# Performance work log

Hardware: AMD Instinct MI355X
Metric: run time of the kernel (lower is better)

## Reference

```python
import jax, jax.numpy as jnp
import numpy as np

NHEADS = 16

def setup_inputs() -> dict:
    key = jax.random.key(0)
    ks = jax.random.split(key, 5)
    C = 1024
    d = C // NHEADS
    x  = jax.random.normal(ks[0], (2, 2048, C), dtype=jnp.float32)
    sc = 1.0 / np.sqrt(C)
    wq = jax.random.normal(ks[1], (C, C), dtype=jnp.float32) * sc
    wk = jax.random.normal(ks[2], (C, C), dtype=jnp.float32) * sc
    wv = jax.random.normal(ks[3], (C, C), dtype=jnp.float32) * sc
    wo = jax.random.normal(ks[4], (d, C), dtype=jnp.float32) * (1.0 / np.sqrt(d))
    return {"x": x, "wq": wq, "wk": wk, "wv": wv, "wo": wo}

def reference(x, wq, wk, wv, wo):
    B, T, C = x.shape
    H = NHEADS
    d = C // H

    def split_heads(y):
        return y.reshape(B, T, H, d).transpose(0, 2, 1, 3)  # [B,H,T,d]

    Q = split_heads(x @ wq)
    K = split_heads(x @ wk)
    V = split_heads(x @ wv)

    # scores[b,h,q,k]
    prod = jnp.einsum('bhqd,bhkd->bhqk', Q, K) / np.sqrt(d)

    # ALiBi bias: offset[h, q, k] = (k - q) * 2**(-8*(h+1)/H)
    idx = jnp.arange(T)
    slopes = jnp.exp2(-8.0 * (jnp.arange(H, dtype=jnp.float32) + 1.0) / H)
    bias = (idx[None, :] - idx[:, None]).astype(x.dtype) * slopes[:, None, None]
    prod = prod + bias[None]

    # causal tril mask: keep k <= q
    keep = idx[None, :] <= idx[:, None]  # [T_q, T_k]
    prod = jnp.where(keep[None, None], prod, -jnp.inf)

    # NOTE: original uses F.softmax(prod, 2) -> softmax over the QUERY axis.
    attention_weights = jax.nn.softmax(prod, axis=2)
    attention_output = jnp.einsum('bhqk,bhkd->bhqd', attention_weights, V)

    # per-head wo projection then sum over heads == (sum over heads) @ wo (linear)
    outputs = attention_output.sum(axis=1) @ wo  # [B,T,C]
    return x + outputs
```

## Files before the change

### kernel.cpp

```cpp
#include <hip/hip_runtime.h>
#include <math.h>

#define NB 2
#define NH 16
#define NT 2048
#define ND 64
#define NC 1024
#define L2E 1.44269504f

typedef __attribute__((ext_vector_type(4))) float f32x4;
typedef __attribute__((ext_vector_type(8))) short short8;
typedef __attribute__((ext_vector_type(4))) short short4_t;
typedef __attribute__((ext_vector_type(8))) unsigned short ushort8;
typedef __attribute__((ext_vector_type(4))) unsigned short ushort4_t;

#define GLOAD_LDS(gp, lp)                                                \
    __builtin_amdgcn_global_load_lds(                                    \
        (const __attribute__((address_space(1))) void*)(gp),             \
        (__attribute__((address_space(3))) void*)(lp), 16, 0, 0)

__device__ __forceinline__ int sigma_p(int p) {
    return 4 * ((p >> 3) & 3) + (p & 3) + 16 * ((p >> 2) & 1) + 32 * (p >> 5);
}

__device__ __forceinline__ unsigned short f2bf(float f) {
    unsigned u = __builtin_bit_cast(unsigned, f);
    unsigned r = (u + 0x7FFFu + ((u >> 16) & 1u)) >> 16;
    return (unsigned short)r;
}

__device__ __forceinline__ unsigned cvtpk_bf16(float lo, float hi) {
    unsigned r;
    asm("v_cvt_pk_bf16_f32 %0, %1, %2" : "=v"(r) : "v"(lo), "v"(hi));
    return r;
}

__device__ __forceinline__ f32x4 mfma16(short8 a, short8 b, f32x4 c) {
    return __builtin_amdgcn_mfma_f32_16x16x32_bf16(a, b, c, 0, 0, 0);
}

__device__ __forceinline__ short8 frag_load(const unsigned short* rowp, int g, int half) {
    short8 v;
    short4_t lo = *(const short4_t*)(rowp + 4 * g + 32 * half);
    short4_t hi = *(const short4_t*)(rowp + 4 * g + 16 + 32 * half);
    #pragma unroll
    for (int j = 0; j < 4; ++j) { v[j] = lo[j]; v[4 + j] = hi[j]; }
    return v;
}

__device__ __forceinline__ short8 frag_g(const unsigned short* rowp, int g, int half) {
    return *(const short8*)(rowp + 8 * g + 32 * half);
}

__device__ __forceinline__ short8 frag_swz128(const unsigned short* tile, int row, int g, int half) {
    const char* p = (const char*)tile + row * 128 + (((g + 4 * half) ^ (row & 7)) << 4);
    return *(const short8*)p;
}

__global__ __launch_bounds__(256) void cvt_x(const float* __restrict__ src,
                                             unsigned short* __restrict__ dst, int n4) {
    int i = blockIdx.x * 256 + threadIdx.x;
    if (i >= n4) return;
    const int blk = i >> 4, c4 = i & 15;
    const int gg = (c4 >> 1) & 3, bb = c4 & 1, hh = c4 >> 3;
    f32x4 v = ((const f32x4*)src)[blk * 16 + gg + 4 * bb + 8 * hh];
    ushort4_t o;
    #pragma unroll
    for (int j = 0; j < 4; ++j) o[j] = f2bf(v[j]);
    ((ushort4_t*)dst)[i] = o;
}

__global__ __launch_bounds__(256) void cvtT3(const float* __restrict__ w0,
                                             const float* __restrict__ w1,
                                             const float* __restrict__ w2,
                                             unsigned short* __restrict__ Wt_all) {
    __shared__ __align__(16) float T[64][68];
    const float* W = (blockIdx.z == 0) ? w0 : ((blockIdx.z == 1) ? w1 : w2);
    unsigned short* Wt = Wt_all + (size_t)blockIdx.z * NC * NC;
    const int tid = threadIdx.x;
    const int k0 = blockIdx.x * 64, n0 = blockIdx.y * 64;
    #pragma unroll
    for (int p = 0; p < 4; ++p) {
        int r = 16 * p + (tid >> 4);
        int c = (tid & 15) * 4;
        *(f32x4*)&T[r][c] = *(const f32x4*)&W[(size_t)(k0 + r) * NC + n0 + c];
    }
    __syncthreads();
    const int nr = tid >> 2, kc = (tid & 3) * 16;
    ushort8 o0, o1;
    #pragma unroll
    for (int j = 0; j < 8; ++j) o0[j] = f2bf(T[sigma_p(kc + j)][nr]);
    #pragma unroll
    for (int j = 0; j < 8; ++j) o1[j] = f2bf(T[sigma_p(kc + 8 + j)][nr]);
    unsigned short* q = Wt + (size_t)(n0 + nr) * NC + k0 + kc;
    *(ushort8*)q       = o0;
    *(ushort8*)(q + 8) = o1;
}

__global__ __launch_bounds__(256) void cvtT_wo(const float* __restrict__ W,
                                               unsigned short* __restrict__ Wt) {
    __shared__ __align__(16) float T[64][68];
    const int tid = threadIdx.x;
    const int n0 = blockIdx.y * 64;
    #pragma unroll
    for (int p = 0; p < 4; ++p) {
        int r = 16 * p + (tid >> 4);
        int c = (tid & 15) * 4;
        *(f32x4*)&T[r][c] = *(const f32x4*)&W[(size_t)r * NC + n0 + c];
    }
    __syncthreads();
    const int nr = tid >> 2, kc = (tid & 3) * 16;
    ushort8 o0, o1;
    #pragma unroll
    for (int j = 0; j < 8; ++j) { o0[j] = f2bf(T[kc + j][nr]); o1[j] = f2bf(T[kc + 8 + j][nr]); }
    unsigned short* q = Wt + (size_t)(n0 + nr) * ND + kc;
    *(ushort8*)q       = o0;
    *(ushort8*)(q + 8) = o1;
}

__global__ __launch_bounds__(256) void gemm_qkv(const unsigned short* __restrict__ Xh,
                                                const unsigned short* __restrict__ Wt_all,
                                                unsigned short* __restrict__ qk_dst,
                                                unsigned short* __restrict__ Vt) {
    __shared__ __align__(16) unsigned short Xs[2][8192];
    __shared__ __align__(16) unsigned short Ws[2][8192];
    const int tid = threadIdx.x;
    const int lane = tid & 63, w = tid >> 6;
    const int g = lane >> 4, l15 = lane & 15;
    const int wr = w >> 1, wc = w & 1;
    const int subrow = lane >> 3;
    const int src_off = (((lane & 7) ^ subrow) << 4);
    const int m0 = blockIdx.x * 128;
    const int which = blockIdx.y >> 3;
    const int n0 = (blockIdx.y & 7) * 128;
    const unsigned short* Wt = Wt_all + (size_t)which * NC * NC;

    f32x4 acc[4][4] = {};

    auto stage = [&](int buf, int kk) {
        #pragma unroll
        for (int i = 0; i < 4; ++i) {
            const int r0 = 8 * w + 32 * i;
            const char* xs = (const char*)Xh + (((size_t)(m0 + r0 + subrow) * NC + kk) << 1) + src_off;
            GLOAD_LDS(xs, (char*)&Xs[buf][r0 * 64]);
            const char* ws = (const char*)Wt + (((size_t)(n0 + r0 + subrow) * NC + kk) << 1) + src_off;
            GLOAD_LDS(ws, (char*)&Ws[buf][r0 * 64]);
        }
    };

    stage(0, 0);
    asm volatile("s_waitcnt vmcnt(0)" ::: "memory");
    __builtin_amdgcn_s_barrier();
    int cur = 0;

    for (int kk = 0; kk < NC; kk += 64) {
        if (kk + 64 < NC) stage(cur ^ 1, kk + 64);
        short8 a[4][2], b[4][2];
        #pragma unroll
        for (int mr = 0; mr < 4; ++mr) {
            a[mr][0] = frag_swz128(Xs[cur], 64 * wr + 16 * mr + l15, g, 0);
            a[mr][1] = frag_swz128(Xs[cur], 64 * wr + 16 * mr + l15, g, 1);
        }
        #pragma unroll
        for (int nc = 0; nc < 4; ++nc) {
            b[nc][0] = frag_swz128(Ws[cur], 64 * wc + 16 * nc + l15, g, 0);
            b[nc][1] = frag_swz128(Ws[cur], 64 * wc + 16 * nc + l15, g, 1);
        }
        #pragma unroll
        for (int mr = 0; mr < 4; ++mr)
            #pragma unroll
            for (int nc = 0; nc < 4; ++nc) {
                acc[mr][nc] = mfma16(a[mr][0], b[nc][0], acc[mr][nc]);
                acc[mr][nc] = mfma16(a[mr][1], b[nc][1], acc[mr][nc]);
            }
        asm volatile("s_waitcnt vmcnt(0)" ::: "memory");
        __builtin_amdgcn_s_barrier();
        cur ^= 1;
    }

    if (which < 2) {
        unsigned short* dst = qk_dst + (size_t)which * (NB * NH * NT * ND);
        #pragma unroll
        for (int mr = 0; mr < 4; ++mr) {
            #pragma unroll
            for (int nc = 0; nc < 4; ++nc) {
                const int n = n0 + 64 * wc + 16 * nc + l15;
                const int hh = n >> 6;
                const int dd = 32 * (nc >> 1) + 8 * (l15 >> 2) + 4 * (nc & 1) + (l15 & 3);
                #pragma unroll
                for (int r = 0; r < 4; ++r) {
                    const int m = m0 + 64 * wr + 16 * mr + 4 * g + r;
                    const int bb = m >> 11, tt = m & (NT - 1);
                    dst[(((size_t)bb * NH + hh) * NT + tt) * ND + dd] = f2bf(acc[mr][nc][r]);
                }
            }
        }
    } else {
        #pragma unroll
        for (int mr = 0; mr < 4; ++mr) {
            const int m = m0 + 64 * wr + 16 * mr + 4 * g;
            const int bb = m >> 11, tt = m & (NT - 1);
            const int tbase = (tt & ~63) + 32 * (mr >> 1) + 8 * g + 4 * (mr & 1);
            #pragma unroll
            for (int nc = 0; nc < 4; ++nc) {
                const int n = n0 + 64 * wc + 16 * nc + l15;
                const int hh = n >> 6, dd = n & 63;
                ushort4_t o;
                #pragma unroll
                for (int r = 0; r < 4; ++r) o[r] = f2bf(acc[mr][nc][r]);
                *(ushort4_t*)&Vt[(((size_t)bb * NH + hh) * ND + dd) * NT + tbase] = o;
            }
        }
    }
}

__global__ __launch_bounds__(256, 4) void colstats(const unsigned short* __restrict__ Qh,
                                                   const unsigned short* __restrict__ Kh,
                                                   float* __restrict__ Lc2) {
    __shared__ __align__(16) unsigned short Qs[3][4096];
    const int tid = threadIdx.x;
    const int lane = tid & 63, w = tid >> 6;
    const int g = lane >> 4, l15 = lane & 15;
    const int subrow = lane >> 3;
    const int src_off = (((lane & 7) ^ subrow) << 4);
    const int lin = blockIdx.x + 32 * blockIdx.y;
    const int xcd = lin & 7, idx = lin >> 3;
    const int bh = xcd * 4 + (idx & 3);
    const int rest = idx >> 2;
    const int j = rest >> 1, par = rest & 1;
    const int jA = j, jB = 31 - j;
    const int hh = bh & (NH - 1);
    const float slL2 = exp2f(-0.5f * (float)(hh + 1)) * L2E;
    const float C1 = 0.125f * L2E;
    const float s16 = 16.f * slL2;

    const int K0A = 64 * jA, K0B = 64 * jB;
    const unsigned short* krA = Kh + ((size_t)bh * NT + K0A + 16 * w + l15) * ND;
    const unsigned short* krB = Kh + ((size_t)bh * NT + K0B + 16 * w + l15) * ND;
    const short8 akA0 = frag_g(krA, g, 0), akA1 = frag_g(krA, g, 1);
    const short8 akB0 = frag_g(krB, g, 0), akB1 = frag_g(krB, g, 1);
    const int kA0 = K0A + 16 * w + 4 * g;
    const int kB0 = K0B + 16 * w + 4 * g;

    const char* Qbase = (const char*)(Qh + (size_t)bh * NT * ND);
    auto stage = [&](int buf, int q0) {
        const char* qs = Qbase + (size_t)(q0 + 16 * w + subrow) * 128 + src_off;
        char* qd = (char*)&Qs[buf][16 * w * 64];
        GLOAD_LDS(qs, qd);
        GLOAD_LDS(qs + 1024, qd + 1024);
    };

    f32x4 accA = {}, accB = {};
    float rs[4];
    #pragma unroll
    for (int r = 0; r < 4; ++r) rs[r] = (float)r * slL2;

    const int qt0 = jA + ((par ^ jA) & 1);
    stage(0, 64 * qt0);
    stage(1, 64 * (qt0 + 2));
    int cur = 0, nxt = 2;

    auto strip = [&](const short8* qf, const short8& a0, const short8& a1,
                     f32x4& acc, float b0, bool mask) {
        #pragma unroll
        for (int q4 = 0; q4 < 4; ++q4) {
            f32x4 d = {};
            __builtin_amdgcn_s_setprio(1);
            d = mfma16(a0, qf[2 * q4], d);
            d = mfma16(a1, qf[2 * q4 + 1], d);
            __builtin_amdgcn_s_setprio(0);
            #pragma unroll
            for (int r = 0; r < 4; ++r) {
                float e = exp2f(fmaf(d[r], C1, b0 + rs[r]));
                if (mask && (16 * q4 + l15 < 16 * w + 4 * g + r)) e = 0.f;
                acc[r] += e;
            }
            b0 -= s16;
        }
    };

    for (int qt = qt0; qt < 32; qt += 2) {
        if (qt + 2 < 32) asm volatile("s_waitcnt vmcnt(2)" ::: "memory");
        else             asm volatile("s_waitcnt vmcnt(0)" ::: "memory");
        __builtin_amdgcn_s_barrier();
        if (qt + 4 < 32) stage(nxt, 64 * (qt + 4));
        const unsigned short* tile = Qs[cur];
        short8 qf[8];
        #pragma unroll
        for (int q4 = 0; q4 < 4; ++q4) {
            qf[2 * q4]     = frag_swz128(tile, 16 * q4 + l15, g, 0);
            qf[2 * q4 + 1] = frag_swz128(tile, 16 * q4 + l15, g, 1);
        }
        const int q0 = 64 * qt;
        strip(qf, akA0, akA1, accA, (float)(kA0 - q0 - l15) * slL2, qt == jA);
        if (qt >= jB)
            strip(qf, akB0, akB1, accB, (float)(kB0 - q0 - l15) * slL2, qt == jB);
        cur = (cur == 2) ? 0 : cur + 1;
        nxt = (nxt == 2) ? 0 : nxt + 1;
    }
    #pragma unroll
    for (int off = 1; off <= 8; off <<= 1) {
        #pragma unroll
        for (int r = 0; r < 4; ++r) {
            accA[r] += __shfl_xor(accA[r], off);
            accB[r] += __shfl_xor(accB[r], off);
        }
    }
    if (l15 == 0) {
        float* Lp = Lc2 + (size_t)(par * 32 + bh) * NT;
        #pragma unroll
        for (int r = 0; r < 4; ++r) {
            Lp[kA0 + r] = accA[r];
            Lp[kB0 + r] = accB[r];
        }
    }
}

__global__ __launch_bounds__(512) void attn_pv(const unsigned short* __restrict__ Qh,
                                               const unsigned short* __restrict__ Kh,
                                               const unsigned short* __restrict__ Vt,
                                               const float* __restrict__ Lc2,
                                               float* __restrict__ att) {
    __shared__ __align__(16) unsigned short Ks[3][4096];
    __shared__ __align__(16) unsigned short Vs[3][4096];
    __shared__ __align__(16) float Ls[NT];
    const int tid = threadIdx.x;
    const int lane = tid & 63, w = tid >> 6;
    const int g = lane >> 4, l15 = lane & 15;
    const int subrow = lane >> 3;
    const int src_off = (((lane & 7) ^ subrow) << 4);
    const int lin = blockIdx.x + 16 * blockIdx.y;
    const int xcd = lin & 7, idx = lin >> 3;
    const int bh = xcd * 4 + (idx & 3);
    const int j = idx >> 2;
    const int jA = j, jB = 31 - j;
    const int hh = bh & (NH - 1);
    const int bb = bh >> 4;
    const float slL2 = exp2f(-0.5f * (float)(hh + 1)) * L2E;
    const float C1 = 0.125f * L2E;

    const bool isB = (w < 4);
    const int wl = isB ? w : (w - 4);
    const int Q0 = isB ? 64 * jB : 64 * jA;
    const int myJ = isB ? jB : jA;
    const int q = Q0 + 16 * wl + l15;

    short8 bq0, bq1;
    {
        const unsigned short* qr = Qh + ((size_t)bh * NT + q) * ND;
        bq0 = frag_g(qr, g, 0);
        bq1 = frag_g(qr, g, 1);
    }

    auto stageKV = [&](int buf, int K0) {
        const char* ksrc = (const char*)Kh + (size_t)((size_t)bh * NT + K0 + 8 * w + subrow) * 128 + src_off;
        GLOAD_LDS(ksrc, (char*)&Ks[buf][8 * w * 64]);
        const char* vsrc = (const char*)Vt + ((((size_t)bh * ND + 8 * w + subrow) * NT + K0) << 1) + src_off;
        GLOAD_LDS(vsrc, (char*)&Vs[buf][8 * w * 64]);
    };

    stageKV(0, 0);
    stageKV(1, 64);
    {
        const f32x4* La = (const f32x4*)(Lc2 + (size_t)bh * NT);
        const f32x4* Lb = (const f32x4*)(Lc2 + (size_t)(32 + bh) * NT);
        const int nv = (jB + 1) * 16;
        for (int i = tid; i < nv; i += 512) {
            f32x4 a = La[i], b = Lb[i];
            float kb = (float)(4 * i);
            f32x4 v;
            #pragma unroll
            for (int c = 0; c < 4; ++c)
                v[c] = log2f(a[c] + b[c]) - (kb + (float)c) * slL2;
            ((f32x4*)Ls)[i] = v;
        }
    }
    asm volatile("s_waitcnt lgkmcnt(0)" ::: "memory");
    int cur = 0, nxt = 2;

    f32x4 o[4] = {};
    const float qsc = (float)q * slL2;

    auto dostrip = [&](const short8* kf, const short8* vf, int K0, bool mask) {
        f32x4 pacc[4];
        __builtin_amdgcn_s_setprio(1);
        #pragma unroll
        for (int s4 = 0; s4 < 4; ++s4) {
            f32x4 d = {};
            d = mfma16(kf[2 * s4], bq0, d);
            d = mfma16(kf[2 * s4 + 1], bq1, d);
            pacc[s4] = d;
        }
        __builtin_amdgcn_s_setprio(0);
        union { unsigned u[4]; short8 s; } pa[2];
        #pragma unroll
        for (int s4 = 0; s4 < 4; ++s4) {
            f32x4 Lf = *(const f32x4*)&Ls[K0 + 16 * s4 + 4 * g];
            float p[4];
            #pragma unroll
            for (int r = 0; r < 4; ++r)
                p[r] = exp2f(fmaf(pacc[s4][r], C1, -(Lf[r] + qsc)));
            if (mask) {
                #pragma unroll
                for (int r = 0; r < 4; ++r)
                    if (K0 + 16 * s4 + 4 * g + r > q) p[r] = 0.f;
            }
            pa[s4 >> 1].u[2 * (s4 & 1)]     = cvtpk_bf16(p[0], p[1]);
            pa[s4 >> 1].u[2 * (s4 & 1) + 1] = cvtpk_bf16(p[2], p[3]);
        }
        __builtin_amdgcn_s_setprio(1);
        #pragma unroll
        for (int n = 0; n < 4; ++n) {
            o[n] = mfma16(pa[0].s, vf[2 * n], o[n]);
            o[n] = mfma16(pa[1].s, vf[2 * n + 1], o[n]);
        }
        __builtin_amdgcn_s_setprio(0);
    };

    for (int kt = 0; kt <= jB; ++kt) {
        if (kt < jB) asm volatile("s_waitcnt vmcnt(2)" ::: "memory");
        else         asm volatile("s_waitcnt vmcnt(0)" ::: "memory");
        __builtin_amdgcn_s_barrier();
        if (kt + 2 <= jB) stageKV(nxt, 64 * (kt + 2));
        if (kt <= myJ) {
            const int K0 = 64 * kt;
            short8 kf[8], vf[8];
            #pragma unroll
            for (int s4 = 0; s4 < 4; ++s4) {
                kf[2 * s4]     = frag_swz128(Ks[cur], 16 * s4 + l15, g, 0);
                kf[2 * s4 + 1] = frag_swz128(Ks[cur], 16 * s4 + l15, g, 1);
                vf[2 * s4]     = frag_swz128(Vs[cur], 16 * s4 + l15, g, 0);
                vf[2 * s4 + 1] = frag_swz128(Vs[cur], 16 * s4 + l15, g, 1);
            }
            dostrip(kf, vf, K0, kt == myJ);
        }
        cur = (cur == 2) ? 0 : cur + 1;
        nxt = (nxt == 2) ? 0 : nxt + 1;
    }
    #pragma unroll
    for (int n = 0; n < 4; ++n) {
        #pragma unroll
        for (int r = 0; r < 4; ++r) {
            att[(((size_t)bb * NT + Q0 + 16 * wl + 4 * g + r) * NH + hh) * ND + 16 * n + l15] = o[n][r];
        }
    }
}

__global__ __launch_bounds__(256) void headsum(const float* __restrict__ att,
                                               unsigned short* __restrict__ A) {
    const int row = blockIdx.x * 16 + (threadIdx.x >> 4);
    const int d0 = (threadIdx.x & 15) * 4;
    const float* p = att + (size_t)row * (NH * ND) + d0;
    f32x4 s = {};
    #pragma unroll
    for (int h = 0; h < NH; ++h)
        s += *(const f32x4*)(p + h * ND);
    ushort4_t o;
    #pragma unroll
    for (int j = 0; j < 4; ++j) o[j] = f2bf(s[j]);
    *(ushort4_t*)&A[(size_t)row * ND + d0] = o;
}

__global__ __launch_bounds__(256) void out_proj(const float* __restrict__ x,
                                                const unsigned short* __restrict__ A,
                                                const unsigned short* __restrict__ Wot,
                                                float* __restrict__ out) {
    const int tid = threadIdx.x;
    const int lane = tid & 63, w = tid >> 6;
    const int g = lane >> 4, l15 = lane & 15;
    const int m0 = blockIdx.x * 64, n0 = blockIdx.y * 64;

    const unsigned short* ar = A + (size_t)(m0 + 16 * w + l15) * ND;
    short8 a0 = frag_load(ar, g, 0);
    short8 a1 = frag_load(ar, g, 1);

    f32x4 acc[4] = {};
    #pragma unroll
    for (int ns = 0; ns < 4; ++ns) {
        const unsigned short* br = Wot + (size_t)(n0 + 16 * ns + l15) * ND;
        acc[ns] = mfma16(a0, frag_load(br, g, 0), acc[ns]);
        acc[ns] = mfma16(a1, frag_load(br, g, 1), acc[ns]);
    }
    #pragma unroll
    for (int ns = 0; ns < 4; ++ns) {
        #pragma unroll
        for (int r = 0; r < 4; ++r) {
            int m = m0 + 16 * w + 4 * g + r;
            int n = n0 + 16 * ns + l15;
            out[(size_t)m * NC + n] = x[(size_t)m * NC + n] + acc[ns][r];
        }
    }
}

extern "C" void kernel_launch(void* const* d_in, const int* in_sizes, int n_in,
                              void* d_out, int out_size, void* d_ws, size_t ws_size,
                              hipStream_t stream) {
    const float* x  = (const float*)d_in[0];
    const float* wq = (const float*)d_in[1];
    const float* wk = (const float*)d_in[2];
    const float* wv = (const float*)d_in[3];
    const float* wo = (const float*)d_in[4];
    float* out = (float*)d_out;

    const size_t MB = 1u << 20;
    const size_t KB = 1u << 10;
    unsigned char* w8 = (unsigned char*)d_ws;
    unsigned short* Xh  = (unsigned short*)(w8);
    unsigned short* Wta = (unsigned short*)(w8 + 8 * MB);
    unsigned short* Qh  = (unsigned short*)(w8 + 16 * MB);
    unsigned short* Kh  = (unsigned short*)(w8 + 24 * MB);
    unsigned short* Vt  = (unsigned short*)(w8 + 32 * MB);
    float*          att = (float*)(w8 + 40 * MB);
    float*          Lc2 = (float*)(w8 + 56 * MB);
    unsigned short* A   = (unsigned short*)(w8 + 56 * MB + 512 * KB);
    unsigned short* Wot = (unsigned short*)(w8 + 57 * MB);

    cvt_x<<<(NB * NT * NC) / 1024, 256, 0, stream>>>(x, Xh, (NB * NT * NC) / 4);
    cvtT3<<<dim3(16, 16, 3), 256, 0, stream>>>(wq, wk, wv, Wta);
    cvtT_wo<<<dim3(1, 16), 256, 0, stream>>>(wo, Wot);

    gemm_qkv<<<dim3(32, 24), 256, 0, stream>>>(Xh, Wta, Qh, Vt);

    colstats<<<dim3(32, 32), 256, 0, stream>>>(Qh, Kh, Lc2);
    attn_pv<<<dim3(16, 32), 512, 0, stream>>>(Qh, Kh, Vt, Lc2, att);

    headsum<<<(NB * NT) / 16, 256, 0, stream>>>(att, A);
    out_proj<<<dim3(64, 16), 256, 0, stream>>>(x, A, Wot, out);
}
```

Before: 141.1 us.

## Fold softmax column normalizer into V and merge weight conversion kernels

The per-key softmax denominator is no longer applied inside the attention loop through a shared-memory log table. A new scale_v kernel instead divides V rows by the column sums ahead of time, and the exponent bias is computed arithmetically from k-q. This removes the LDS table build, its log2 work and the per-strip LDS reads from attn_pv, at the cost of an extra pass over V and an extra bf16 rounding of the scaled V. The wo conversion is also merged into the QKV weight conversion launch, which saves one launch but adds many early-exiting blocks.

```diff
diff --git a/kernel.cpp b/kernel.cpp
--- a/kernel.cpp
+++ b/kernel.cpp
@@ -27,6 +27,10 @@
     unsigned u = __builtin_bit_cast(unsigned, f);
     unsigned r = (u + 0x7FFFu + ((u >> 16) & 1u)) >> 16;
     return (unsigned short)r;
+}
+
+__device__ __forceinline__ float bf2f(unsigned short s) {
+    return __builtin_bit_cast(float, (unsigned)s << 16);
 }
 
 __device__ __forceinline__ unsigned cvtpk_bf16(float lo, float hi) {
@@ -70,14 +74,36 @@
     ((ushort4_t*)dst)[i] = o;
 }
 
-__global__ __launch_bounds__(256) void cvtT3(const float* __restrict__ w0,
-                                             const float* __restrict__ w1,
-                                             const float* __restrict__ w2,
-                                             unsigned short* __restrict__ Wt_all) {
+__global__ __launch_bounds__(256) void cvtW(const float* __restrict__ w0,
+                                            const float* __restrict__ w1,
+                                            const float* __restrict__ w2,
+                                            const float* __restrict__ w3,
+                                            unsigned short* __restrict__ Wt_all,
+                                            unsigned short* __restrict__ Wot) {
     __shared__ __align__(16) float T[64][68];
-    const float* W = (blockIdx.z == 0) ? w0 : ((blockIdx.z == 1) ? w1 : w2);
-    unsigned short* Wt = Wt_all + (size_t)blockIdx.z * NC * NC;
+    const int z = blockIdx.z;
     const int tid = threadIdx.x;
+    if (z == 3) {
+        if (blockIdx.x != 0) return;
+        const int n0 = blockIdx.y * 64;
+        #pragma unroll
+        for (int p = 0; p < 4; ++p) {
+            int r = 16 * p + (tid >> 4);
+            int c = (tid & 15) * 4;
+            *(f32x4*)&T[r][c] = *(const f32x4*)&w3[(size_t)r * NC + n0 + c];
+        }
+        __syncthreads();
+        const int nr = tid >> 2, kc = (tid & 3) * 16;
+        ushort8 o0, o1;
+        #pragma unroll
+        for (int j = 0; j < 8; ++j) { o0[j] = f2bf(T[kc + j][nr]); o1[j] = f2bf(T[kc + 8 + j][nr]); }
+        unsigned short* q = Wot + (size_t)(n0 + nr) * ND + kc;
+        *(ushort8*)q       = o0;
+        *(ushort8*)(q + 8) = o1;
+        return;
+    }
+    const float* W = (z == 0) ? w0 : ((z == 1) ? w1 : w2);
+    unsigned short* Wt = Wt_all + (size_t)z * NC * NC;
     const int k0 = blockIdx.x * 64, n0 = blockIdx.y * 64;
     #pragma unroll
     for (int p = 0; p < 4; ++p) {
@@ -93,27 +119,6 @@
     #pragma unroll
     for (int j = 0; j < 8; ++j) o1[j] = f2bf(T[sigma_p(kc + 8 + j)][nr]);
     unsigned short* q = Wt + (size_t)(n0 + nr) * NC + k0 + kc;
-    *(ushort8*)q       = o0;
-    *(ushort8*)(q + 8) = o1;
-}
-
-__global__ __launch_bounds__(256) void cvtT_wo(const float* __restrict__ W,
-                                               unsigned short* __restrict__ Wt) {
-    __shared__ __align__(16) float T[64][68];
-    const int tid = threadIdx.x;
-    const int n0 = blockIdx.y * 64;
-    #pragma unroll
-    for (int p = 0; p < 4; ++p) {
-        int r = 16 * p + (tid >> 4);
-        int c = (tid & 15) * 4;
-        *(f32x4*)&T[r][c] = *(const f32x4*)&W[(size_t)r * NC + n0 + c];
-    }
-    __syncthreads();
-    const int nr = tid >> 2, kc = (tid & 3) * 16;
-    ushort8 o0, o1;
-    #pragma unroll
-    for (int j = 0; j < 8; ++j) { o0[j] = f2bf(T[kc + j][nr]); o1[j] = f2bf(T[kc + 8 + j][nr]); }
-    unsigned short* q = Wt + (size_t)(n0 + nr) * ND + kc;
     *(ushort8*)q       = o0;
     *(ushort8*)(q + 8) = o1;
 }
@@ -316,14 +321,30 @@
     }
 }
 
+__global__ __launch_bounds__(256) void scale_v(const float* __restrict__ Lc2,
+                                               unsigned short* __restrict__ Vt) {
+    const int i = blockIdx.x * 256 + threadIdx.x;
+    const int bh = i >> 15;
+    const int tpos4 = (i & 511) * 4;
+    const int tlog = (tpos4 & ~63) + sigma_p(tpos4 & 63);
+    const float* Sa = Lc2 + (size_t)bh * NT + tlog;
+    const float* Sb = Lc2 + (size_t)(32 + bh) * NT + tlog;
+    f32x4 a = *(const f32x4*)Sa;
+    f32x4 b = *(const f32x4*)Sb;
+    ushort4_t v = ((const ushort4_t*)Vt)[i];
+    ushort4_t o;
+    #pragma unroll
+    for (int j = 0; j < 4; ++j)
+        o[j] = f2bf(bf2f(v[j]) / (a[j] + b[j]));
+    ((ushort4_t*)Vt)[i] = o;
+}
+
 __global__ __launch_bounds__(512) void attn_pv(const unsigned short* __restrict__ Qh,
                                                const unsigned short* __restrict__ Kh,
                                                const unsigned short* __restrict__ Vt,
-                                               const float* __restrict__ Lc2,
                                                float* __restrict__ att) {
     __shared__ __align__(16) unsigned short Ks[3][4096];
     __shared__ __align__(16) unsigned short Vs[3][4096];
-    __shared__ __align__(16) float Ls[NT];
     const int tid = threadIdx.x;
     const int lane = tid & 63, w = tid >> 6;
     const int g = lane >> 4, l15 = lane & 15;
@@ -338,6 +359,7 @@
     const int bb = bh >> 4;
     const float slL2 = exp2f(-0.5f * (float)(hh + 1)) * L2E;
     const float C1 = 0.125f * L2E;
+    const float s16 = 16.f * slL2;
 
     const bool isB = (w < 4);
     const int wl = isB ? w : (w - 4);
@@ -351,6 +373,9 @@
         bq0 = frag_g(qr, g, 0);
         bq1 = frag_g(qr, g, 1);
     }
+    float rs[4];
+    #pragma unroll
+    for (int r = 0; r < 4; ++r) rs[r] = (float)r * slL2;
 
     auto stageKV = [&](int buf, int K0) {
         const char* ksrc = (const char*)Kh + (size_t)((size_t)bh * NT + K0 + 8 * w + subrow) * 128 + src_off;
@@ -361,25 +386,9 @@
 
     stageKV(0, 0);
     stageKV(1, 64);
-    {
-        const f32x4* La = (const f32x4*)(Lc2 + (size_t)bh * NT);
-        const f32x4* Lb = (const f32x4*)(Lc2 + (size_t)(32 + bh) * NT);
-        const int nv = (jB + 1) * 16;
-        for (int i = tid; i < nv; i += 512) {
-            f32x4 a = La[i], b = Lb[i];
-            float kb = (float)(4 * i);
-            f32x4 v;
-            #pragma unroll
-            for (int c = 0; c < 4; ++c)
-                v[c] = log2f(a[c] + b[c]) - (kb + (float)c) * slL2;
-            ((f32x4*)Ls)[i] = v;
-        }
-    }
-    asm volatile("s_waitcnt lgkmcnt(0)" ::: "memory");
     int cur = 0, nxt = 2;
 
     f32x4 o[4] = {};
-    const float qsc = (float)q * slL2;
 
     auto dostrip = [&](const short8* kf, const short8* vf, int K0, bool mask) {
         f32x4 pacc[4];
@@ -393,13 +402,13 @@
         }
         __builtin_amdgcn_s_setprio(0);
         union { unsigned u[4]; short8 s; } pa[2];
+        float b = (float)(K0 + 4 * g - q) * slL2;
         #pragma unroll
         for (int s4 = 0; s4 < 4; ++s4) {
-            f32x4 Lf = *(const f32x4*)&Ls[K0 + 16 * s4 + 4 * g];
             float p[4];
             #pragma unroll
             for (int r = 0; r < 4; ++r)
-                p[r] = exp2f(fmaf(pacc[s4][r], C1, -(Lf[r] + qsc)));
+                p[r] = exp2f(fmaf(pacc[s4][r], C1, b + rs[r]));
             if (mask) {
                 #pragma unroll
                 for (int r = 0; r < 4; ++r)
@@ -407,6 +416,7 @@
             }
             pa[s4 >> 1].u[2 * (s4 & 1)]     = cvtpk_bf16(p[0], p[1]);
             pa[s4 >> 1].u[2 * (s4 & 1) + 1] = cvtpk_bf16(p[2], p[3]);
+            b += s16;
         }
         __builtin_amdgcn_s_setprio(1);
         #pragma unroll
@@ -516,13 +526,13 @@
     unsigned short* Wot = (unsigned short*)(w8 + 57 * MB);
 
     cvt_x<<<(NB * NT * NC) / 1024, 256, 0, stream>>>(x, Xh, (NB * NT * NC) / 4);
-    cvtT3<<<dim3(16, 16, 3), 256, 0, stream>>>(wq, wk, wv, Wta);
-    cvtT_wo<<<dim3(1, 16), 256, 0, stream>>>(wo, Wot);
+    cvtW<<<dim3(16, 16, 4), 256, 0, stream>>>(wq, wk, wv, wo, Wta, Wot);
 
     gemm_qkv<<<dim3(32, 24), 256, 0, stream>>>(Xh, Wta, Qh, Vt);
 
     colstats<<<dim3(32, 32), 256, 0, stream>>>(Qh, Kh, Lc2);
-    attn_pv<<<dim3(16, 32), 512, 0, stream>>>(Qh, Kh, Vt, Lc2, att);
+    scale_v<<<(32 * ND * NT / 4) / 256, 256, 0, stream>>>(Lc2, Vt);
+    attn_pv<<<dim3(16, 32), 512, 0, stream>>>(Qh, Kh, Vt, att);
 
     headsum<<<(NB * NT) / 16, 256, 0, stream>>>(att, A);
     out_proj<<<dim3(64, 16), 256, 0, stream>>>(x, A, Wot, out);
```

Result: no change. 142.6 us (+1.0%).
